# Performance work log

Measured on AMD Instinct MI355X. Metric: run time of the kernel, lower is better.

The kernel has to match this reference:

```python
import jax, jax.numpy as jnp
import numpy as np

NQ, NC, E, D, HID = 131072, 65536, 1048576, 128, 256
LN_EPS = 1e-5


def _ln(x, g, b):
    m = jnp.mean(x, axis=-1, keepdims=True)
    v = jnp.mean((x - m) ** 2, axis=-1, keepdims=True)
    return (x - m) * jax.lax.rsqrt(v + LN_EPS) * g + b


def _safe_inv_sqrt(x):
    # x^{-1/2} where x > 0, else 0 (matches _safe_inv_sqrt in torch code)
    return jnp.where(x > 0, jax.lax.rsqrt(jnp.where(x > 0, x, 1.0)), 0.0)


def setup_inputs() -> dict:
    key = jax.random.key(0)
    ks = jax.random.split(key, 24)
    s = 1.0 / np.sqrt(D)
    inp = {}
    inp['H_Q'] = jax.random.normal(ks[0], (NQ, D), jnp.float32)
    inp['H_C'] = jax.random.normal(ks[1], (NC, D), jnp.float32)
    eQC_src = jax.random.randint(ks[2], (E,), 0, NQ, jnp.int32)
    eQC_dst = jax.random.randint(ks[3], (E,), 0, NC, jnp.int32)
    eCQ_src = jax.random.randint(ks[4], (E,), 0, NC, jnp.int32)
    eCQ_dst = jax.random.randint(ks[5], (E,), 0, NQ, jnp.int32)
    inp['eQC_src'], inp['eQC_dst'] = eQC_src, eQC_dst
    inp['eCQ_src'], inp['eCQ_dst'] = eCQ_src, eCQ_dst
    ones = jnp.ones((E,), jnp.float32)
    inp['deg_QC_src'] = jax.ops.segment_sum(ones, eQC_src, num_segments=NQ)
    inp['deg_QC_dst'] = jax.ops.segment_sum(ones, eQC_dst, num_segments=NC)
    inp['deg_CQ_src'] = jax.ops.segment_sum(ones, eCQ_src, num_segments=NC)
    inp['deg_CQ_dst'] = jax.ops.segment_sum(ones, eCQ_dst, num_segments=NQ)
    for t, i in (('Q', 6), ('C', 7)):
        inp[f'ln_g_{t}'] = jnp.ones((D,), jnp.float32)
        inp[f'ln_b_{t}'] = jnp.zeros((D,), jnp.float32)
        inp[f'Wres_{t}'] = jax.random.normal(ks[i], (D, D), jnp.float32) * s
    inp['Wrel_QC'] = jax.random.normal(ks[8], (D, D), jnp.float32) * s
    inp['Wrel_CQ'] = jax.random.normal(ks[9], (D, D), jnp.float32) * s
    inp['gate_QC'] = jnp.ones((), jnp.float32)
    inp['gate_CQ'] = jnp.ones((), jnp.float32)
    for t, i in (('Q', 10), ('C', 12)):
        inp[f'W1_{t}'] = jax.random.normal(ks[i], (2 * D, HID), jnp.float32) * (1.0 / np.sqrt(2 * D))
        inp[f'b1_{t}'] = jnp.zeros((HID,), jnp.float32)
        inp[f'W2_{t}'] = jax.random.normal(ks[i + 1], (HID, D), jnp.float32) * (1.0 / np.sqrt(HID))
        inp[f'b2_{t}'] = jnp.zeros((D,), jnp.float32)
    return inp


def _spmm_sym(X_src, e_src, e_dst, deg_src, deg_dst, n_dst):
    # symmetric-normalized SpMM: D_dst^{-1/2} A D_src^{-1/2} X
    Xn = X_src * _safe_inv_sqrt(deg_src)[:, None]
    msg = jax.ops.segment_sum(Xn[e_src], e_dst, num_segments=n_dst)
    return msg * _safe_inv_sqrt(deg_dst)[:, None]


def _update(proj, agg, W1, b1, W2, b2):
    h = jax.nn.gelu(jnp.concatenate([proj, agg], axis=-1) @ W1 + b1, approximate=False)
    return proj + (h @ W2 + b2)  # residual=True, dropout=0 (eval)


def reference(H_Q, H_C, eQC_src, eQC_dst, eCQ_src, eCQ_dst,
              deg_QC_src, deg_QC_dst, deg_CQ_src, deg_CQ_dst,
              ln_g_Q, ln_b_Q, ln_g_C, ln_b_C, Wres_Q, Wres_C,
              Wrel_QC, Wrel_CQ, gate_QC, gate_CQ,
              W1_Q, b1_Q, W2_Q, b2_Q, W1_C, b1_C, W2_C, b2_C):
    projQ = _ln(H_Q, ln_g_Q, ln_b_Q) @ Wres_Q
    projC = _ln(H_C, ln_g_C, ln_b_C) @ Wres_C
    # relation Q_C: src=Q, dst=C
    msgC = _spmm_sym(H_Q @ Wrel_QC, eQC_src, eQC_dst, deg_QC_src, deg_QC_dst, NC) * gate_QC
    # relation C_Q: src=C, dst=Q
    msgQ = _spmm_sym(H_C @ Wrel_CQ, eCQ_src, eCQ_dst, deg_CQ_src, deg_CQ_dst, NQ) * gate_CQ
    outQ = _update(projQ, msgQ, W1_Q, b1_Q, W2_Q, b2_Q)
    outC = _update(projC, msgC, W1_C, b1_C, W2_C, b2_C)
    return (outQ, outC)
```

## Files before the change

kernel.cpp:

```cpp
#include <hip/hip_runtime.h>
#include <stdint.h>

#define NQn 131072
#define NCn 65536
#define En  1048576

typedef __bf16 bf16;
typedef __bf16 bf16x2 __attribute__((ext_vector_type(2)));
typedef __bf16 bf16x4 __attribute__((ext_vector_type(4)));
typedef __bf16 bf16x8 __attribute__((ext_vector_type(8)));
typedef float  f32x4  __attribute__((ext_vector_type(4)));

__global__ void wtrans_all(
    const float* __restrict__ w0, bf16* __restrict__ t0,
    const float* __restrict__ w1, bf16* __restrict__ t1,
    const float* __restrict__ w2, bf16* __restrict__ t2,
    const float* __restrict__ w3, bf16* __restrict__ t3,
    const float* __restrict__ w4, bf16* __restrict__ t4,
    const float* __restrict__ w5, bf16* __restrict__ t5,
    const float* __restrict__ w6, bf16* __restrict__ t6,
    const float* __restrict__ w7, bf16* __restrict__ t7) {
  const float* W; bf16* T; int K, M;
  switch (blockIdx.y) {
    case 0: W = w0; T = t0; K = 128; M = 128; break;
    case 1: W = w1; T = t1; K = 128; M = 128; break;
    case 2: W = w2; T = t2; K = 128; M = 128; break;
    case 3: W = w3; T = t3; K = 128; M = 128; break;
    case 4: W = w4; T = t4; K = 256; M = 256; break;
    case 5: W = w5; T = t5; K = 256; M = 256; break;
    case 6: W = w6; T = t6; K = 256; M = 128; break;
    default: W = w7; T = t7; K = 256; M = 128; break;
  }
  int t = blockIdx.x * 256 + threadIdx.x;
  if (t >= K * M) return;
  int KB = K >> 5;
  int frag = t >> 9, within = t & 511;
  int lane = within >> 3, j = within & 7;
  int mb = frag / KB, kb = frag % KB;
  int m = mb * 16 + (lane & 15);
  int k = kb * 32 + (lane >> 4) * 8 + j;
  T[t] = (bf16)W[k * M + m];
}

__global__ __launch_bounds__(256, 5) void dual_gemm2(
    const float* __restrict__ HQ, const float* __restrict__ lngQ,
    const float* __restrict__ lnbQ, const bf16* __restrict__ WresQ,
    const bf16* __restrict__ WrelQ, const float* __restrict__ degQ,
    bf16* __restrict__ projQ, bf16* __restrict__ xnQ, int splitQ,
    const float* __restrict__ HC, const float* __restrict__ lngC,
    const float* __restrict__ lnbC, const bf16* __restrict__ WresC,
    const bf16* __restrict__ WrelC, const float* __restrict__ degC,
    bf16* __restrict__ projC, bf16* __restrict__ xnC) {
  __shared__ __align__(16) unsigned char lds[32768];
  const float *H, *lng, *lnb, *degsrc;
  const bf16 *Wres, *Wrel;
  bf16 *proj, *xn;
  int bid = blockIdx.x;
  if (bid < splitQ) {
    H = HQ; lng = lngQ; lnb = lnbQ; Wres = WresQ; Wrel = WrelQ;
    degsrc = degQ; proj = projQ; xn = xnQ;
  } else {
    bid -= splitQ;
    H = HC; lng = lngC; lnb = lnbC; Wres = WresC; Wrel = WrelC;
    degsrc = degC; proj = projC; xn = xnC;
  }
  const int tid = threadIdx.x;
  const int row0 = bid * 64;
  const int wid = tid >> 6, lane = tid & 63;
  const int wrow = (wid >> 1) * 32, wcol = (wid & 1) * 64;

  #pragma unroll
  for (int it = 0; it < 8; ++it) {
    int lin = it * 256 + tid;
    int r = lin >> 5;
    int c = (lin & 31) * 4;
    float4 v = *(const float4*)(H + (size_t)(row0 + r) * 128 + c);
    float s = v.x + v.y + v.z + v.w;
    #pragma unroll
    for (int o = 16; o; o >>= 1) s += __shfl_xor(s, o, 64);
    float mean = s * (1.0f / 128.0f);
    float d0 = v.x - mean, d1 = v.y - mean, d2 = v.z - mean, d3 = v.w - mean;
    float q = d0 * d0 + d1 * d1 + d2 * d2 + d3 * d3;
    #pragma unroll
    for (int o = 16; o; o >>= 1) q += __shfl_xor(q, o, 64);
    float rsv = rsqrtf(q * (1.0f / 128.0f) + 1e-5f);
    float4 gg = *(const float4*)(lng + c);
    float4 bb = *(const float4*)(lnb + c);
    bf16x4 w;
    w[0] = (bf16)(d0 * rsv * gg.x + bb.x);
    w[1] = (bf16)(d1 * rsv * gg.y + bb.y);
    w[2] = (bf16)(d2 * rsv * gg.z + bb.z);
    w[3] = (bf16)(d3 * rsv * gg.w + bb.w);
    int off = r * 256 + ((c * 2) ^ ((r & 7) << 4));
    *(bf16x4*)(lds + off) = w;
    bf16x4 rw;
    rw[0] = (bf16)v.x; rw[1] = (bf16)v.y; rw[2] = (bf16)v.z; rw[3] = (bf16)v.w;
    *(bf16x4*)(lds + 16384 + off) = rw;
  }
  __syncthreads();

  const int rloc = wrow + (lane >> 4) * 4;
  const int cloc = wcol + (lane & 15);

  {
    f32x4 acc[2][4] = {};
    #pragma unroll
    for (int kk = 0; kk < 4; ++kk) {
      const int kb = kk * 64 + (lane >> 4) * 16;
      bf16x8 af[2], bfv[4];
      #pragma unroll
      for (int fc = 0; fc < 4; ++fc) {
        int cblk = (wid & 1) * 4 + fc;
        bfv[fc] = *(const bf16x8*)(Wres + ((size_t)(cblk * 4 + kk) * 64 + lane) * 8);
      }
      #pragma unroll
      for (int fr = 0; fr < 2; ++fr) {
        int ar = wrow + fr * 16 + (lane & 15);
        af[fr] = *(const bf16x8*)(lds + ar * 256 + (kb ^ ((ar & 7) << 4)));
      }
      #pragma unroll
      for (int fr = 0; fr < 2; ++fr)
        #pragma unroll
        for (int fc = 0; fc < 4; ++fc)
          acc[fr][fc] = __builtin_amdgcn_mfma_f32_16x16x32_bf16(
              af[fr], bfv[fc], acc[fr][fc], 0, 0, 0);
    }
    __syncthreads();
    #pragma unroll
    for (int fr = 0; fr < 2; ++fr)
      #pragma unroll
      for (int fc = 0; fc < 4; ++fc)
        #pragma unroll
        for (int r = 0; r < 4; ++r) {
          int row = rloc + fr * 16 + r;
          int colb = (cloc + fc * 16) * 2;
          *(bf16*)(lds + row * 256 + (colb ^ ((row & 7) << 4))) =
              (bf16)acc[fr][fc][r];
        }
  }

  {
    f32x4 acc[2][4] = {};
    #pragma unroll
    for (int kk = 0; kk < 4; ++kk) {
      const int kb = kk * 64 + (lane >> 4) * 16;
      bf16x8 af[2], bfv[4];
      #pragma unroll
      for (int fc = 0; fc < 4; ++fc) {
        int cblk = (wid & 1) * 4 + fc;
        bfv[fc] = *(const bf16x8*)(Wrel + ((size_t)(cblk * 4 + kk) * 64 + lane) * 8);
      }
      #pragma unroll
      for (int fr = 0; fr < 2; ++fr) {
        int ar = wrow + fr * 16 + (lane & 15);
        af[fr] = *(const bf16x8*)(lds + 16384 + ar * 256 + (kb ^ ((ar & 7) << 4)));
      }
      #pragma unroll
      for (int fr = 0; fr < 2; ++fr)
        #pragma unroll
        for (int fc = 0; fc < 4; ++fc)
          acc[fr][fc] = __builtin_amdgcn_mfma_f32_16x16x32_bf16(
              af[fr], bfv[fc], acc[fr][fc], 0, 0, 0);
    }
    __syncthreads();
    #pragma unroll
    for (int fr = 0; fr < 2; ++fr) {
      float rs[4];
      #pragma unroll
      for (int r = 0; r < 4; ++r) {
        float dv = degsrc[row0 + rloc + fr * 16 + r];
        rs[r] = dv > 0.f ? rsqrtf(dv) : 0.f;
      }
      #pragma unroll
      for (int fc = 0; fc < 4; ++fc)
        #pragma unroll
        for (int r = 0; r < 4; ++r) {
          int row = rloc + fr * 16 + r;
          int colb = (cloc + fc * 16) * 2;
          *(bf16*)(lds + 16384 + row * 256 + (colb ^ ((row & 7) << 4))) =
              (bf16)(acc[fr][fc][r] * rs[r]);
        }
    }
  }
  __syncthreads();

  #pragma unroll
  for (int it = 0; it < 8; ++it) {
    int lin = it * 256 + tid;
    int pb = (lin < 1024) ? 0 : 16384;
    bf16* dst = (lin < 1024) ? proj : xn;
    int chunk = lin & 1023;
    int r = chunk >> 4;
    int cb = (chunk & 15) * 16;
    bf16x8 v = *(const bf16x8*)(lds + pb + r * 256 + (cb ^ ((r & 7) << 4)));
    *(bf16x8*)((char*)(dst + (size_t)(row0 + r) * 128) + cb) = v;
  }
}

__global__ __launch_bounds__(256, 4) void mlp_fused2(
    const bf16* __restrict__ projQ, const bf16* __restrict__ msgQ,
    const bf16* __restrict__ W1Q, const float* __restrict__ b1Q,
    const bf16* __restrict__ W2Q, const float* __restrict__ b2Q,
    float* __restrict__ outQ, int splitQ,
    const bf16* __restrict__ projC, const bf16* __restrict__ msgC,
    const bf16* __restrict__ W1C, const float* __restrict__ b1C,
    const bf16* __restrict__ W2C, const float* __restrict__ b2C,
    float* __restrict__ outC) {
  __shared__ __align__(16) unsigned char lds[32768];
  const bf16 *proj, *msg, *W1p, *W2p;
  const float *b1, *b2;
  float* out;
  int bid = blockIdx.x;
  if (bid < splitQ) {
    proj = projQ; msg = msgQ; W1p = W1Q; b1 = b1Q; W2p = W2Q; b2 = b2Q; out = outQ;
  } else {
    bid -= splitQ;
    proj = projC; msg = msgC; W1p = W1C; b1 = b1C; W2p = W2C; b2 = b2C; out = outC;
  }
  const int tid = threadIdx.x;
  const int row0 = bid * 64;
  const int wid = tid >> 6, lane = tid & 63;

  #pragma unroll
  for (int it = 0; it < 8; ++it) {
    int lin = it * 256 + tid;
    int r = lin >> 5;
    int cb = (lin & 31) * 16;
    const bf16* src = (cb < 256) ? (proj + (size_t)(row0 + r) * 128)
                                 : (msg + (size_t)(row0 + r) * 128 - 128);
    bf16x8 v = *(const bf16x8*)((const char*)src + cb);
    *(bf16x8*)(lds + r * 512 + (cb ^ ((r & 7) << 4))) = v;
  }
  __syncthreads();

  f32x4 acc1[4][4] = {};
  #pragma unroll
  for (int kk = 0; kk < 8; ++kk) {
    const int kb = kk * 64 + (lane >> 4) * 16;
    bf16x8 af[4], bfv[4];
    #pragma unroll
    for (int fc = 0; fc < 4; ++fc) {
      int cblk = wid * 4 + fc;
      bfv[fc] = *(const bf16x8*)(W1p + ((size_t)(cblk * 8 + kk) * 64 + lane) * 8);
    }
    #pragma unroll
    for (int fr = 0; fr < 4; ++fr) {
      int ar = fr * 16 + (lane & 15);
      af[fr] = *(const bf16x8*)(lds + ar * 512 + (kb ^ ((ar & 7) << 4)));
    }
    #pragma unroll
    for (int fr = 0; fr < 4; ++fr)
      #pragma unroll
      for (int fc = 0; fc < 4; ++fc)
        acc1[fr][fc] = __builtin_amdgcn_mfma_f32_16x16x32_bf16(
            af[fr], bfv[fc], acc1[fr][fc], 0, 0, 0);
  }
  __syncthreads();

  {
    const int rb = (lane >> 4) * 4;
    const int cb0 = wid * 64 + (lane & 15);
    #pragma unroll
    for (int fc = 0; fc < 4; ++fc) {
      int col = cb0 + fc * 16;
      float bv = b1[col];
      #pragma unroll
      for (int fr = 0; fr < 4; ++fr) {
        #pragma unroll
        for (int r = 0; r < 4; ++r) {
          int row = rb + fr * 16 + r;
          float x = acc1[fr][fc][r] + bv;
          float u2 = 1.5957691216057308f * (x + 0.044715f * x * x * x);
          float e = __expf(u2);
          x = 0.5f * x * (1.f + (1.f - 2.f / (e + 1.f)));
          *(bf16*)(lds + row * 512 + ((col * 2) ^ ((row & 7) << 4))) = (bf16)x;
        }
      }
    }
  }
  __syncthreads();

  const int wrow2 = (wid >> 1) * 32;
  const int wcol2 = (wid & 1) * 64;
  f32x4 acc2[2][4] = {};
  #pragma unroll
  for (int kk = 0; kk < 8; ++kk) {
    const int kb = kk * 64 + (lane >> 4) * 16;
    bf16x8 af[2], bfv[4];
    #pragma unroll
    for (int fc = 0; fc < 4; ++fc) {
      int cblk = (wid & 1) * 4 + fc;
      bfv[fc] = *(const bf16x8*)(W2p + ((size_t)(cblk * 8 + kk) * 64 + lane) * 8);
    }
    #pragma unroll
    for (int fr = 0; fr < 2; ++fr) {
      int ar = wrow2 + fr * 16 + (lane & 15);
      af[fr] = *(const bf16x8*)(lds + ar * 512 + (kb ^ ((ar & 7) << 4)));
    }
    #pragma unroll
    for (int fr = 0; fr < 2; ++fr)
      #pragma unroll
      for (int fc = 0; fc < 4; ++fc)
        acc2[fr][fc] = __builtin_amdgcn_mfma_f32_16x16x32_bf16(
            af[fr], bfv[fc], acc2[fr][fc], 0, 0, 0);
  }
  const int rbase = wrow2 + (lane >> 4) * 4;
  const int cbase = wcol2 + (lane & 15);
  #pragma unroll
  for (int fr = 0; fr < 2; ++fr) {
    #pragma unroll
    for (int fc = 0; fc < 4; ++fc) {
      int col = cbase + fc * 16;
      float bv = b2[col];
      #pragma unroll
      for (int r = 0; r < 4; ++r) {
        int row = row0 + rbase + fr * 16 + r;
        out[(size_t)row * 128 + col] =
            acc2[fr][fc][r] + bv + (float)proj[(size_t)row * 128 + col];
      }
    }
  }
}

__global__ __launch_bounds__(256) void bucket_hist(
    const float* __restrict__ degQC, const float* __restrict__ degCQ,
    int* __restrict__ bcnt) {
  int w = (blockIdx.x * 256 + threadIdx.x) >> 6;
  int lane = threadIdx.x & 63;
  const float* deg = (w < 512) ? (degQC + (size_t)w * 128)
                               : (degCQ + (size_t)(w - 512) * 128);
  float s = deg[lane] + deg[lane + 64];
  #pragma unroll
  for (int o = 32; o; o >>= 1) s += __shfl_xor(s, o, 64);
  if (lane == 0) bcnt[w] = (int)(s + 0.5f);
}

__global__ __launch_bounds__(1024) void bucket_scan(
    const int* __restrict__ bcnt,
    int* __restrict__ baseQC, int* __restrict__ gcurQC,
    int* __restrict__ baseCQ, int* __restrict__ gcurCQ) {
  __shared__ int ss[1024];
  const int t = threadIdx.x;
  int v = (t < 512) ? bcnt[t] : 0;
  ss[t] = v;
  __syncthreads();
  for (int o = 1; o < 1024; o <<= 1) {
    int x = (t >= o) ? ss[t - o] : 0;
    __syncthreads();
    ss[t] += x;
    __syncthreads();
  }
  if (t < 512) { int e = ss[t] - v; baseQC[t] = e; gcurQC[t] = e; }
  if (t == 0) baseQC[512] = En;
  __syncthreads();
  int v2 = bcnt[512 + t];
  ss[t] = v2;
  __syncthreads();
  for (int o = 1; o < 1024; o <<= 1) {
    int x = (t >= o) ? ss[t - o] : 0;
    __syncthreads();
    ss[t] += x;
    __syncthreads();
  }
  { int e = ss[t] - v2; baseCQ[t] = e; gcurCQ[t] = e; }
  if (t == 0) baseCQ[1024] = En;
}

#define CHUNK 4096

__global__ __launch_bounds__(256) void bucketA2(
    const int* __restrict__ esrcQ, const int* __restrict__ edstQ,
    int* __restrict__ gcurQ, uint2* __restrict__ ebufQ, int splitQ,
    const int* __restrict__ esrcC, const int* __restrict__ edstC,
    int* __restrict__ gcurC, uint2* __restrict__ ebufC) {
  constexpr int NB = 1024;
  __shared__ int lcount[NB], lexcl[NB], lbase[NB], lofs[NB];
  __shared__ int ss[256];
  __shared__ uint2 stage[CHUNK];
  const int* esrc; const int* edst; int* gcur; uint2* ebuf; int nb;
  int bid = blockIdx.x;
  if (bid < splitQ) { esrc = esrcQ; edst = edstQ; gcur = gcurQ; ebuf = ebufQ; nb = 512; }
  else { bid -= splitQ; esrc = esrcC; edst = edstC; gcur = gcurC; ebuf = ebufC; nb = 1024; }
  const int t = threadIdx.x;
  for (int b = t; b < NB; b += 256) lcount[b] = 0;
  __syncthreads();
  const int e0 = bid * CHUNK;
  uint2 ed[16];
  #pragma unroll
  for (int j = 0; j < 16; ++j) {
    int e = e0 + j * 256 + t;
    ed[j].x = (unsigned)esrc[e];
    ed[j].y = (unsigned)edst[e];
    atomicAdd(&lcount[ed[j].y >> 7], 1);
  }
  __syncthreads();
  int c[4]; int mysum = 0;
  #pragma unroll
  for (int j = 0; j < 4; ++j) { c[j] = lcount[t * 4 + j]; mysum += c[j]; }
  ss[t] = mysum;
  __syncthreads();
  for (int o = 1; o < 256; o <<= 1) {
    int x = (t >= o) ? ss[t - o] : 0;
    __syncthreads();
    ss[t] += x;
    __syncthreads();
  }
  int run = ss[t] - mysum;
  #pragma unroll
  for (int j = 0; j < 4; ++j) { lexcl[t * 4 + j] = run; run += c[j]; }
  __syncthreads();
  for (int b = t; b < NB; b += 256) {
    lbase[b] = (b < nb && lcount[b]) ? atomicAdd(&gcur[b], lcount[b]) : 0;
    lofs[b]  = lexcl[b];
  }
  __syncthreads();
  #pragma unroll
  for (int j = 0; j < 16; ++j) {
    int b = ed[j].y >> 7;
    int p = atomicAdd(&lofs[b], 1);
    stage[p] = ed[j];
  }
  __syncthreads();
  for (int i = t; i < CHUNK; i += 256) {
    uint2 v = stage[i];
    int b = v.y >> 7;
    ebuf[lbase[b] + (i - lexcl[b])] = v;
  }
}

__global__ __launch_bounds__(256) void bucketB22(
    const uint2* __restrict__ ebufQ, const int* __restrict__ bbaseQ,
    const float* __restrict__ degQ, int* __restrict__ offsQ,
    int* __restrict__ csrQ, int splitQ,
    const uint2* __restrict__ ebufC, const int* __restrict__ bbaseC,
    const float* __restrict__ degC, int* __restrict__ offsC,
    int* __restrict__ csrC) {
  __shared__ int sdeg[128];
  __shared__ int lcur[128];
  const uint2* ebuf; const int* bbase; const float* degdst; int* offs; int* csr;
  int b = blockIdx.x;
  if (b < splitQ) { ebuf = ebufQ; bbase = bbaseQ; degdst = degQ; offs = offsQ; csr = csrQ; }
  else { b -= splitQ; ebuf = ebufC; bbase = bbaseC; degdst = degC; offs = offsC; csr = csrC; }
  const int t = threadIdx.x;
  const int base = bbase[b], end = bbase[b + 1];
  int myv = 0;
  if (t < 128) {
    myv = (int)(degdst[(size_t)b * 128 + t] + 0.5f);
    sdeg[t] = myv;
  }
  __syncthreads();
  for (int o = 1; o < 128; o <<= 1) {
    int x = (t < 128 && t >= o) ? sdeg[t - o] : 0;
    __syncthreads();
    if (t < 128) sdeg[t] += x;
    __syncthreads();
  }
  if (t < 128) {
    int excl = sdeg[t] - myv;
    lcur[t] = excl;
    offs[(size_t)b * 128 + t] = base + excl;
  }
  __syncthreads();
  for (int i = base + t; i < end; i += 256) {
    uint2 v = ebuf[i];
    int p = atomicAdd(&lcur[v.y & 127], 1);
    csr[base + p] = (int)v.x;
  }
}

__global__ __launch_bounds__(256) void gather_one(
    const bf16* __restrict__ Xn, const int* __restrict__ csr,
    const int* __restrict__ offs, const float* __restrict__ degdst,
    const float* __restrict__ gate, bf16* __restrict__ msg) {
  int d = blockIdx.x * 4 + (threadIdx.x >> 6);
  int lane = threadIdx.x & 63;
  int half = lane >> 5, sl = lane & 31;
  float dv = degdst[d];
  int cnt = (int)(dv + 0.5f);
  int start = offs[d];
  float a0 = 0.f, a1 = 0.f, a2 = 0.f, a3 = 0.f;
  int i = 0;
  for (; i + 8 <= cnt; i += 8) {
    int s0 = csr[start + i + half * 4 + 0];
    int s1 = csr[start + i + half * 4 + 1];
    int s2 = csr[start + i + half * 4 + 2];
    int s3 = csr[start + i + half * 4 + 3];
    bf16x4 v0 = *(const bf16x4*)(Xn + (size_t)s0 * 128 + sl * 4);
    bf16x4 v1 = *(const bf16x4*)(Xn + (size_t)s1 * 128 + sl * 4);
    bf16x4 v2 = *(const bf16x4*)(Xn + (size_t)s2 * 128 + sl * 4);
    bf16x4 v3 = *(const bf16x4*)(Xn + (size_t)s3 * 128 + sl * 4);
    a0 += (float)v0[0] + (float)v1[0] + (float)v2[0] + (float)v3[0];
    a1 += (float)v0[1] + (float)v1[1] + (float)v2[1] + (float)v3[1];
    a2 += (float)v0[2] + (float)v1[2] + (float)v2[2] + (float)v3[2];
    a3 += (float)v0[3] + (float)v1[3] + (float)v2[3] + (float)v3[3];
  }
  for (; i + 2 <= cnt; i += 2) {
    int s0 = csr[start + i + half];
    bf16x4 v0 = *(const bf16x4*)(Xn + (size_t)s0 * 128 + sl * 4);
    a0 += (float)v0[0]; a1 += (float)v0[1];
    a2 += (float)v0[2]; a3 += (float)v0[3];
  }
  if (i < cnt && half == 0) {
    int s0 = csr[start + i];
    bf16x4 v0 = *(const bf16x4*)(Xn + (size_t)s0 * 128 + sl * 4);
    a0 += (float)v0[0]; a1 += (float)v0[1];
    a2 += (float)v0[2]; a3 += (float)v0[3];
  }
  a0 += __shfl_xor(a0, 32, 64);
  a1 += __shfl_xor(a1, 32, 64);
  a2 += __shfl_xor(a2, 32, 64);
  a3 += __shfl_xor(a3, 32, 64);
  if (half == 0) {
    float sc = (dv > 0.f ? rsqrtf(dv) : 0.f) * gate[0];
    bf16x4 r;
    r[0] = (bf16)(a0 * sc); r[1] = (bf16)(a1 * sc);
    r[2] = (bf16)(a2 * sc); r[3] = (bf16)(a3 * sc);
    *(bf16x4*)(msg + (size_t)d * 128 + sl * 4) = r;
  }
}

extern "C" void kernel_launch(void* const* d_in, const int* in_sizes, int n_in,
                              void* d_out, int out_size, void* d_ws, size_t ws_size,
                              hipStream_t stream) {
  const float* H_Q        = (const float*)d_in[0];
  const float* H_C        = (const float*)d_in[1];
  const int*   eQC_src    = (const int*)d_in[2];
  const int*   eQC_dst    = (const int*)d_in[3];
  const int*   eCQ_src    = (const int*)d_in[4];
  const int*   eCQ_dst    = (const int*)d_in[5];
  const float* deg_QC_src = (const float*)d_in[6];
  const float* deg_QC_dst = (const float*)d_in[7];
  const float* deg_CQ_src = (const float*)d_in[8];
  const float* deg_CQ_dst = (const float*)d_in[9];
  const float* ln_g_Q     = (const float*)d_in[10];
  const float* ln_b_Q     = (const float*)d_in[11];
  const float* Wres_Q     = (const float*)d_in[12];
  const float* ln_g_C     = (const float*)d_in[13];
  const float* ln_b_C     = (const float*)d_in[14];
  const float* Wres_C     = (const float*)d_in[15];
  const float* Wrel_QC    = (const float*)d_in[16];
  const float* Wrel_CQ    = (const float*)d_in[17];
  const float* gate_QC    = (const float*)d_in[18];
  const float* gate_CQ    = (const float*)d_in[19];
  const float* W1_Q       = (const float*)d_in[20];
  const float* b1_Q       = (const float*)d_in[21];
  const float* W2_Q       = (const float*)d_in[22];
  const float* b2_Q       = (const float*)d_in[23];
  const float* W1_C       = (const float*)d_in[24];
  const float* b1_C       = (const float*)d_in[25];
  const float* W2_C       = (const float*)d_in[26];
  const float* b2_C       = (const float*)d_in[27];

  char* ws = (char*)d_ws;
  size_t o = 0;
  auto alloc = [&](size_t bytes) -> char* {
    char* p = ws + o;
    o += (bytes + 255) & ~(size_t)255;
    return p;
  };
  bf16* xnbQ = (bf16*)alloc((size_t)NQn * 128 * 2);
  bf16* xnbC = (bf16*)alloc((size_t)NCn * 128 * 2);
  int*  csrQC = (int*)alloc((size_t)En * 4);
  int*  csrCQ = (int*)alloc((size_t)En * 4);
  bf16* projQ = (bf16*)alloc((size_t)NQn * 128 * 2);
  bf16* projC = (bf16*)alloc((size_t)NCn * 128 * 2);
  bf16* msgQ  = (bf16*)alloc((size_t)NQn * 128 * 2);
  bf16* msgC  = (bf16*)alloc((size_t)NCn * 128 * 2);
  uint2* ebufQC = (uint2*)alloc((size_t)En * 8);
  uint2* ebufCQ = (uint2*)alloc((size_t)En * 8);
  bf16* WresQt = (bf16*)alloc(128 * 128 * 2);
  bf16* WresCt = (bf16*)alloc(128 * 128 * 2);
  bf16* WrelQCt = (bf16*)alloc(128 * 128 * 2);
  bf16* WrelCQt = (bf16*)alloc(128 * 128 * 2);
  bf16* W1Qt = (bf16*)alloc(256 * 256 * 2);
  bf16* W1Ct = (bf16*)alloc(256 * 256 * 2);
  bf16* W2Qt = (bf16*)alloc(128 * 256 * 2);
  bf16* W2Ct = (bf16*)alloc(128 * 256 * 2);
  int* bcnt   = (int*)alloc(1536 * 4);
  int* bbaseQC = (int*)alloc(513 * 4);
  int* bbaseCQ = (int*)alloc(1025 * 4);
  int* gcurQC = (int*)alloc(512 * 4);
  int* gcurCQ = (int*)alloc(1024 * 4);
  int* offsQC = (int*)alloc((size_t)NCn * 4);
  int* offsCQ = (int*)alloc((size_t)NQn * 4);

  float* outQ = (float*)d_out;
  float* outC = (float*)d_out + (size_t)NQn * 128;

  wtrans_all<<<dim3(256, 8), 256, 0, stream>>>(
      Wres_Q, WresQt, Wres_C, WresCt, Wrel_QC, WrelQCt, Wrel_CQ, WrelCQt,
      W1_Q, W1Qt, W1_C, W1Ct, W2_Q, W2Qt, W2_C, W2Ct);
  bucket_hist<<<384, 256, 0, stream>>>(deg_QC_dst, deg_CQ_dst, bcnt);
  bucket_scan<<<1, 1024, 0, stream>>>(bcnt, bbaseQC, gcurQC, bbaseCQ, gcurCQ);

  bucketA2<<<512, 256, 0, stream>>>(eQC_src, eQC_dst, gcurQC, ebufQC, 256,
                                    eCQ_src, eCQ_dst, gcurCQ, ebufCQ);
  bucketB22<<<1536, 256, 0, stream>>>(ebufQC, bbaseQC, deg_QC_dst, offsQC,
                                      csrQC, 512,
                                      ebufCQ, bbaseCQ, deg_CQ_dst, offsCQ,
                                      csrCQ);

  dual_gemm2<<<NQn / 64 + NCn / 64, 256, 0, stream>>>(
      H_Q, ln_g_Q, ln_b_Q, WresQt, WrelQCt, deg_QC_src, projQ, xnbQ, NQn / 64,
      H_C, ln_g_C, ln_b_C, WresCt, WrelCQt, deg_CQ_src, projC, xnbC);

  gather_one<<<NQn / 4, 256, 0, stream>>>(xnbC, csrCQ, offsCQ, deg_CQ_dst,
                                          gate_CQ, msgQ);
  gather_one<<<NCn / 4, 256, 0, stream>>>(xnbQ, csrQC, offsQC, deg_QC_dst,
                                          gate_QC, msgC);

  mlp_fused2<<<NQn / 64 + NCn / 64, 256, 0, stream>>>(
      projQ, msgQ, W1Qt, b1_Q, W2Qt, b2_Q, outQ, NQn / 64,
      projC, msgC, W1Ct, b1_C, W2Ct, b2_C, outC);
}
```

Baseline: 277.3 us.

## Fuse edge bucketing pass into dual GEMM kernel as extra blocks

Merges the independent bucketA edge-partitioning kernel and the LayerNorm+dual-projection GEMM kernel into one launch, with block ranges dispatching to either workload. Bucket chunks shrink from 4096 to 2048 edges so the shared LDS buffer fits both roles. The goal is to overlap memory-bound scatter work with GEMM tiles and remove a launch. The cost is more bucketing blocks, more global atomics on gcur, and occupancy now set by the larger shared-memory footprint with launch bounds of 4 instead of 5.

```diff
diff --git a/kernel.cpp b/kernel.cpp
--- a/kernel.cpp
+++ b/kernel.cpp
@@ -42,28 +42,12 @@
   T[t] = (bf16)W[k * M + m];
 }
 
-__global__ __launch_bounds__(256, 5) void dual_gemm2(
-    const float* __restrict__ HQ, const float* __restrict__ lngQ,
-    const float* __restrict__ lnbQ, const bf16* __restrict__ WresQ,
-    const bf16* __restrict__ WrelQ, const float* __restrict__ degQ,
-    bf16* __restrict__ projQ, bf16* __restrict__ xnQ, int splitQ,
-    const float* __restrict__ HC, const float* __restrict__ lngC,
-    const float* __restrict__ lnbC, const bf16* __restrict__ WresC,
-    const bf16* __restrict__ WrelC, const float* __restrict__ degC,
-    bf16* __restrict__ projC, bf16* __restrict__ xnC) {
-  __shared__ __align__(16) unsigned char lds[32768];
-  const float *H, *lng, *lnb, *degsrc;
-  const bf16 *Wres, *Wrel;
-  bf16 *proj, *xn;
-  int bid = blockIdx.x;
-  if (bid < splitQ) {
-    H = HQ; lng = lngQ; lnb = lnbQ; Wres = WresQ; Wrel = WrelQ;
-    degsrc = degQ; proj = projQ; xn = xnQ;
-  } else {
-    bid -= splitQ;
-    H = HC; lng = lngC; lnb = lnbC; Wres = WresC; Wrel = WrelC;
-    degsrc = degC; proj = projC; xn = xnC;
-  }
+__device__ __forceinline__ void dual_tile(
+    unsigned char* lds, int bid,
+    const float* __restrict__ H, const float* __restrict__ lng,
+    const float* __restrict__ lnb, const bf16* __restrict__ Wres,
+    const bf16* __restrict__ Wrel, const float* __restrict__ degsrc,
+    bf16* __restrict__ proj, bf16* __restrict__ xn) {
   const int tid = threadIdx.x;
   const int row0 = bid * 64;
   const int wid = tid >> 6, lane = tid & 63;
@@ -194,6 +178,89 @@
     int cb = (chunk & 15) * 16;
     bf16x8 v = *(const bf16x8*)(lds + pb + r * 256 + (cb ^ ((r & 7) << 4)));
     *(bf16x8*)((char*)(dst + (size_t)(row0 + r) * 128) + cb) = v;
+  }
+}
+
+__device__ __forceinline__ void bucketA_chunk(
+    unsigned char* ldsraw, int chunk,
+    const int* __restrict__ esrc, const int* __restrict__ edst,
+    int* __restrict__ gcur, uint2* __restrict__ ebuf, int nb) {
+  int* lcount = (int*)ldsraw;
+  int* lexcl  = (int*)(ldsraw + 4096);
+  int* lbase  = (int*)(ldsraw + 8192);
+  int* lofs   = (int*)(ldsraw + 12288);
+  int* ss     = (int*)(ldsraw + 16384);
+  uint2* stage = (uint2*)(ldsraw + 17408);
+  const int t = threadIdx.x;
+  for (int b = t; b < 1024; b += 256) lcount[b] = 0;
+  __syncthreads();
+  const int e0 = chunk * 2048;
+  uint2 ed[8];
+  #pragma unroll
+  for (int j = 0; j < 8; ++j) {
+    int e = e0 + j * 256 + t;
+    ed[j].x = (unsigned)esrc[e];
+    ed[j].y = (unsigned)edst[e];
+    atomicAdd(&lcount[ed[j].y >> 7], 1);
+  }
+  __syncthreads();
+  int c[4]; int mysum = 0;
+  #pragma unroll
+  for (int j = 0; j < 4; ++j) { c[j] = lcount[t * 4 + j]; mysum += c[j]; }
+  ss[t] = mysum;
+  __syncthreads();
+  for (int o = 1; o < 256; o <<= 1) {
+    int x = (t >= o) ? ss[t - o] : 0;
+    __syncthreads();
+    ss[t] += x;
+    __syncthreads();
+  }
+  int run = ss[t] - mysum;
+  #pragma unroll
+  for (int j = 0; j < 4; ++j) { lexcl[t * 4 + j] = run; run += c[j]; }
+  __syncthreads();
+  for (int b = t; b < 1024; b += 256) {
+    lbase[b] = (b < nb && lcount[b]) ? atomicAdd(&gcur[b], lcount[b]) : 0;
+    lofs[b]  = lexcl[b];
+  }
+  __syncthreads();
+  #pragma unroll
+  for (int j = 0; j < 8; ++j) {
+    int b = ed[j].y >> 7;
+    int p = atomicAdd(&lofs[b], 1);
+    stage[p] = ed[j];
+  }
+  __syncthreads();
+  for (int i = t; i < 2048; i += 256) {
+    uint2 v = stage[i];
+    int b = v.y >> 7;
+    ebuf[lbase[b] + (i - lexcl[b])] = v;
+  }
+}
+
+__global__ __launch_bounds__(256, 4) void fusedA(
+    const float* __restrict__ HQ, const float* __restrict__ lngQ,
+    const float* __restrict__ lnbQ, const bf16* __restrict__ WresQ,
+    const bf16* __restrict__ WrelQ, const float* __restrict__ degQ,
+    bf16* __restrict__ projQ, bf16* __restrict__ xnQ,
+    const float* __restrict__ HC, const float* __restrict__ lngC,
+    const float* __restrict__ lnbC, const bf16* __restrict__ WresC,
+    const bf16* __restrict__ WrelC, const float* __restrict__ degC,
+    bf16* __restrict__ projC, bf16* __restrict__ xnC,
+    const int* __restrict__ eQCs, const int* __restrict__ eQCd,
+    int* __restrict__ gcurQC, uint2* __restrict__ ebufQC,
+    const int* __restrict__ eCQs, const int* __restrict__ eCQd,
+    int* __restrict__ gcurCQ, uint2* __restrict__ ebufCQ) {
+  __shared__ __align__(16) unsigned char lds[33792];
+  int bid = blockIdx.x;
+  if (bid < 2048) {
+    dual_tile(lds, bid, HQ, lngQ, lnbQ, WresQ, WrelQ, degQ, projQ, xnQ);
+  } else if (bid < 3072) {
+    dual_tile(lds, bid - 2048, HC, lngC, lnbC, WresC, WrelC, degC, projC, xnC);
+  } else if (bid < 3584) {
+    bucketA_chunk(lds, bid - 3072, eQCs, eQCd, gcurQC, ebufQC, 512);
+  } else {
+    bucketA_chunk(lds, bid - 3584, eCQs, eCQd, gcurCQ, ebufCQ, 1024);
   }
 }
 
@@ -364,68 +431,6 @@
   }
   { int e = ss[t] - v2; baseCQ[t] = e; gcurCQ[t] = e; }
   if (t == 0) baseCQ[1024] = En;
-}
-
-#define CHUNK 4096
-
-__global__ __launch_bounds__(256) void bucketA2(
-    const int* __restrict__ esrcQ, const int* __restrict__ edstQ,
-    int* __restrict__ gcurQ, uint2* __restrict__ ebufQ, int splitQ,
-    const int* __restrict__ esrcC, const int* __restrict__ edstC,
-    int* __restrict__ gcurC, uint2* __restrict__ ebufC) {
-  constexpr int NB = 1024;
-  __shared__ int lcount[NB], lexcl[NB], lbase[NB], lofs[NB];
-  __shared__ int ss[256];
-  __shared__ uint2 stage[CHUNK];
-  const int* esrc; const int* edst; int* gcur; uint2* ebuf; int nb;
-  int bid = blockIdx.x;
-  if (bid < splitQ) { esrc = esrcQ; edst = edstQ; gcur = gcurQ; ebuf = ebufQ; nb = 512; }
-  else { bid -= splitQ; esrc = esrcC; edst = edstC; gcur = gcurC; ebuf = ebufC; nb = 1024; }
-  const int t = threadIdx.x;
-  for (int b = t; b < NB; b += 256) lcount[b] = 0;
-  __syncthreads();
-  const int e0 = bid * CHUNK;
-  uint2 ed[16];
-  #pragma unroll
-  for (int j = 0; j < 16; ++j) {
-    int e = e0 + j * 256 + t;
-    ed[j].x = (unsigned)esrc[e];
-    ed[j].y = (unsigned)edst[e];
-    atomicAdd(&lcount[ed[j].y >> 7], 1);
-  }
-  __syncthreads();
-  int c[4]; int mysum = 0;
-  #pragma unroll
-  for (int j = 0; j < 4; ++j) { c[j] = lcount[t * 4 + j]; mysum += c[j]; }
-  ss[t] = mysum;
-  __syncthreads();
-  for (int o = 1; o < 256; o <<= 1) {
-    int x = (t >= o) ? ss[t - o] : 0;
-    __syncthreads();
-    ss[t] += x;
-    __syncthreads();
-  }
-  int run = ss[t] - mysum;
-  #pragma unroll
-  for (int j = 0; j < 4; ++j) { lexcl[t * 4 + j] = run; run += c[j]; }
-  __syncthreads();
-  for (int b = t; b < NB; b += 256) {
-    lbase[b] = (b < nb && lcount[b]) ? atomicAdd(&gcur[b], lcount[b]) : 0;
-    lofs[b]  = lexcl[b];
-  }
-  __syncthreads();
-  #pragma unroll
-  for (int j = 0; j < 16; ++j) {
-    int b = ed[j].y >> 7;
-    int p = atomicAdd(&lofs[b], 1);
-    stage[p] = ed[j];
-  }
-  __syncthreads();
-  for (int i = t; i < CHUNK; i += 256) {
-    uint2 v = stage[i];
-    int b = v.y >> 7;
-    ebuf[lbase[b] + (i - lexcl[b])] = v;
-  }
 }
 
 __global__ __launch_bounds__(256) void bucketB22(
@@ -593,17 +598,17 @@
   bucket_hist<<<384, 256, 0, stream>>>(deg_QC_dst, deg_CQ_dst, bcnt);
   bucket_scan<<<1, 1024, 0, stream>>>(bcnt, bbaseQC, gcurQC, bbaseCQ, gcurCQ);
 
-  bucketA2<<<512, 256, 0, stream>>>(eQC_src, eQC_dst, gcurQC, ebufQC, 256,
-                                    eCQ_src, eCQ_dst, gcurCQ, ebufCQ);
+  fusedA<<<4096, 256, 0, stream>>>(
+      H_Q, ln_g_Q, ln_b_Q, WresQt, WrelQCt, deg_QC_src, projQ, xnbQ,
+      H_C, ln_g_C, ln_b_C, WresCt, WrelCQt, deg_CQ_src, projC, xnbC,
+      eQC_src, eQC_dst, gcurQC, ebufQC,
+      eCQ_src, eCQ_dst, gcurCQ, ebufCQ);
+
   bucketB22<<<1536, 256, 0, stream>>>(ebufQC, bbaseQC, deg_QC_dst, offsQC,
                                       csrQC, 512,
                                       ebufCQ, bbaseCQ, deg_CQ_dst, offsCQ,
                                       csrCQ);
 
-  dual_gemm2<<<NQn / 64 + NCn / 64, 256, 0, stream>>>(
-      H_Q, ln_g_Q, ln_b_Q, WresQt, WrelQCt, deg_QC_src, projQ, xnbQ, NQn / 64,
-      H_C, ln_g_C, ln_b_C, WresCt, WrelCQt, deg_CQ_src, projC, xnbC);
-
   gather_one<<<NQn / 4, 256, 0, stream>>>(xnbC, csrCQ, offsCQ, deg_CQ_dst,
                                           gate_CQ, msgQ);
   gather_one<<<NCn / 4, 256, 0, stream>>>(xnbQ, csrQC, offsQC, deg_QC_dst,
```

Result: faster. 265.1 us (-4.4%).
